# Optimization experiments

Measured on AMD Instinct MI355X. Metric: run time of the kernel, lower is better.

## Reference

```python
import jax, jax.numpy as jnp
import numpy as np

B, S, D, H = 2, 2048, 1024, 16
DH = D // H  # depth per head = 64


def setup_inputs() -> dict:
    key = jax.random.key(0)
    ks = jax.random.split(key, 5)
    sc = 0.02
    return {
        "x": jax.random.normal(ks[0], (B, S, D), dtype=jnp.float32),
        "Wq": jax.random.normal(ks[1], (D, D), dtype=jnp.float32) * sc,
        "bq": jnp.zeros((D,), dtype=jnp.float32),
        "Wk": jax.random.normal(ks[2], (D, D), dtype=jnp.float32) * sc,
        "bk": jnp.zeros((D,), dtype=jnp.float32),
        "Wv": jax.random.normal(ks[3], (D, D), dtype=jnp.float32) * sc,
        "bv": jnp.zeros((D,), dtype=jnp.float32),
        "Wo": jax.random.normal(ks[4], (D, D), dtype=jnp.float32) * sc,
        "bo": jnp.zeros((D,), dtype=jnp.float32),
    }


def _split_heads(t):
    # [B,S,D] -> [B,H,S,DH]
    return t.reshape(B, S, H, DH).transpose(0, 2, 1, 3)


def reference(x, Wq, bq, Wk, bk, Wv, bv, Wo, bo):
    q = _split_heads(x @ Wq + bq)
    k = _split_heads(x @ Wk + bk)
    v = _split_heads(x @ Wv + bv)
    scale = 1.0 / jnp.sqrt(jnp.float32(DH))
    logits = jnp.einsum("bhqd,bhkd->bhqk", q, k) * scale  # [B,H,S,S]
    attn = jax.nn.softmax(logits, axis=-1)
    ctx = jnp.einsum("bhqk,bhkd->bhqd", attn, v)
    ctx = ctx.transpose(0, 2, 1, 3).reshape(B, S, D)
    # dropout is identity at inference
    return ctx @ Wo + bo
```

## Files before the change

kernel.cpp:

```cpp
#include <hip/hip_runtime.h>
#include <hip/hip_bf16.h>

#define S_LEN   2048
#define D_MODEL 1024
#define NHEAD   16
#define DHEAD   64
#define M_ROWS  4096
#define BHEADS  32
#define MEG     1048576

typedef __attribute__((ext_vector_type(8)))  short short8;
typedef __attribute__((ext_vector_type(4)))  float f32x4;
typedef __attribute__((ext_vector_type(16))) float f32x16;
typedef __attribute__((ext_vector_type(4)))  unsigned short us4;
typedef __attribute__((ext_vector_type(2)))  unsigned int uint2v;
typedef __attribute__((ext_vector_type(4)))  unsigned int uint4v;

extern "C" __device__ float __ocml_native_exp2_f32(float);

__device__ __forceinline__ unsigned short f2b(float f) {
    unsigned int u = __builtin_bit_cast(unsigned int, f);
    return (unsigned short)((u + 0x7FFFu + ((u >> 16) & 1u)) >> 16);
}

__device__ __forceinline__ unsigned int cvtpk(float lo, float hi) {
    unsigned int r;
    asm("v_cvt_pk_bf16_f32 %0, %1, %2" : "=v"(r) : "v"(lo), "v"(hi));
    return r;
}

__device__ __forceinline__ float b2f(unsigned short b) {
    return __builtin_bit_cast(float, (unsigned int)b << 16);
}

#define GLOAD16(gp, lp) __builtin_amdgcn_global_load_lds(                     \
        (const __attribute__((address_space(1))) void*)(gp),                  \
        (__attribute__((address_space(3))) void*)(lp), 16, 0, 0)

#define STAGE_OFS(lane) ((((lane) & 3) ^ (((lane) >> 3) & 3)) * 8)

#define ZERO16(v) do { _Pragma("unroll")                                      \
    for (int z_ = 0; z_ < 16; ++z_) (v)[z_] = 0.f; } while (0)

__global__ __launch_bounds__(256) void prep(
    const float* __restrict__ x, unsigned short* __restrict__ xb,
    const float* __restrict__ Wq, const float* __restrict__ Wk,
    const float* __restrict__ Wv, const float* __restrict__ Wo,
    unsigned short* __restrict__ Wqt, unsigned short* __restrict__ Wkt,
    unsigned short* __restrict__ Wvt, unsigned short* __restrict__ Wot)
{
    const int z = blockIdx.z;
    const int tx = threadIdx.x, ty = threadIdx.y;
    if (z == 4) {
        const int blk = blockIdx.y * 32 + blockIdx.x;
        const int base = (blk * 256 + ty * 32 + tx) * 4;
        #pragma unroll
        for (int r = 0; r < 4; ++r) {
            const int i = base + r * (M_ROWS * D_MODEL / 4);
            const float4 v = *(const float4*)&x[i];
            us4 o;
            o.x = f2b(v.x); o.y = f2b(v.y); o.z = f2b(v.z); o.w = f2b(v.w);
            *(us4*)&xb[i] = o;
        }
        return;
    }
    __shared__ float tile[32][33];
    const float* W = z == 0 ? Wq : (z == 1 ? Wk : (z == 2 ? Wv : Wo));
    unsigned short* Wt = z == 0 ? Wqt : (z == 1 ? Wkt : (z == 2 ? Wvt : Wot));
    const int n0 = blockIdx.x * 32, k0 = blockIdx.y * 32;
    #pragma unroll
    for (int i = 0; i < 4; ++i)
        tile[ty + i * 8][tx] = W[(size_t)(k0 + ty + i * 8) * D_MODEL + n0 + tx];
    __syncthreads();
    #pragma unroll
    for (int i = 0; i < 4; ++i)
        Wt[(size_t)(n0 + ty + i * 8) * D_MODEL + k0 + tx] = f2b(tile[tx][ty + i * 8]);
}

__global__ __launch_bounds__(256) void gemm_qkv(
    const unsigned short* __restrict__ xb,
    const unsigned short* __restrict__ Wqt, const unsigned short* __restrict__ Wkt,
    const unsigned short* __restrict__ Wvt,
    const float* __restrict__ bq, const float* __restrict__ bk,
    const float* __restrict__ bv,
    unsigned short* __restrict__ Qb, unsigned short* __restrict__ Kb,
    unsigned short* __restrict__ Vt)
{
    __shared__ unsigned short As[2][128][32];
    __shared__ unsigned short Bs[2][128][32];

    const int id  = (blockIdx.z * 32 + blockIdx.y) * 8 + blockIdx.x;
    const int swz = (id & 7) * 96 + (id >> 3);
    const int z   = swz >> 8;
    const int rem = swz & 255;
    const int bm  = (rem >> 3) * 128;
    const int bn  = (rem & 7) * 128;

    const unsigned short* Wt = z == 0 ? Wqt : (z == 1 ? Wkt : Wvt);
    const float* bias = z == 0 ? bq : (z == 1 ? bk : bv);

    const int t = threadIdx.x, lane = t & 63, w = t >> 6;
    const int wm = w >> 1, wn = w & 1;
    const int lr = lane >> 2, lc = STAGE_OFS(lane);
    const int lm = lane & 15, quad = lane >> 4;
    const int qo = (quad ^ ((lm >> 1) & 3)) * 8;

    f32x4 acc[4][4] = {};

    #pragma unroll
    for (int i = 0; i < 2; ++i) {
        const int c = 2 * w + i;
        GLOAD16(xb + (size_t)(bm + c * 16 + lr) * D_MODEL + lc, &As[0][c * 16][0]);
        GLOAD16(Wt + (size_t)(bn + c * 16 + lr) * D_MODEL + lc, &Bs[0][c * 16][0]);
    }
    __syncthreads();

    for (int it = 0; it < 32; ++it) {
        const int cur = it & 1;
        if (it + 1 < 32) {
            const int kt = (it + 1) * 32;
            #pragma unroll
            for (int i = 0; i < 2; ++i) {
                const int c = 2 * w + i;
                GLOAD16(xb + (size_t)(bm + c * 16 + lr) * D_MODEL + kt + lc,
                        &As[cur ^ 1][c * 16][0]);
                GLOAD16(Wt + (size_t)(bn + c * 16 + lr) * D_MODEL + kt + lc,
                        &Bs[cur ^ 1][c * 16][0]);
            }
        }

        short8 af[4], bfr[4];
        #pragma unroll
        for (int mi = 0; mi < 4; ++mi)
            af[mi] = *(const short8*)&As[cur][wm * 64 + mi * 16 + lm][qo];
        #pragma unroll
        for (int ni = 0; ni < 4; ++ni)
            bfr[ni] = *(const short8*)&Bs[cur][wn * 64 + ni * 16 + lm][qo];
        #pragma unroll
        for (int mi = 0; mi < 4; ++mi)
            #pragma unroll
            for (int ni = 0; ni < 4; ++ni)
                acc[mi][ni] = __builtin_amdgcn_mfma_f32_16x16x32_bf16(
                    af[mi], bfr[ni], acc[mi][ni], 0, 0, 0);

        __syncthreads();
    }

    float bb[4];
    #pragma unroll
    for (int ni = 0; ni < 4; ++ni)
        bb[ni] = bias[bn + wn * 64 + ni * 16 + lm];
    const float scale = (z == 0) ? 0.18033688011112042f : 1.0f;

    if (z < 2) {
        unsigned short* Out = (z == 0) ? Qb : Kb;
        #pragma unroll
        for (int mi = 0; mi < 4; ++mi)
            #pragma unroll
            for (int r = 0; r < 4; ++r) {
                const int row = bm + wm * 64 + mi * 16 + quad * 4 + r;
                const int b = row >> 11, s = row & 2047;
                #pragma unroll
                for (int ni = 0; ni < 4; ++ni) {
                    const int col = bn + wn * 64 + ni * 16 + lm;
                    const int h = col >> 6, d = col & 63;
                    Out[(((size_t)(b * NHEAD + h)) * S_LEN + s) * DHEAD + d] =
                        f2b((acc[mi][ni][r] + bb[ni]) * scale);
                }
            }
    } else {
        #pragma unroll
        for (int mi = 0; mi < 4; ++mi) {
            const int row0 = bm + wm * 64 + mi * 16 + quad * 4;
            const int b = row0 >> 11, s0 = row0 & 2047;
            #pragma unroll
            for (int ni = 0; ni < 4; ++ni) {
                const int col = bn + wn * 64 + ni * 16 + lm;
                const int h = col >> 6, d = col & 63;
                us4 pk;
                pk.x = f2b(acc[mi][ni][0] + bb[ni]);
                pk.y = f2b(acc[mi][ni][1] + bb[ni]);
                pk.z = f2b(acc[mi][ni][2] + bb[ni]);
                pk.w = f2b(acc[mi][ni][3] + bb[ni]);
                *(us4*)&Vt[(((size_t)(b * NHEAD + h)) * DHEAD + d) * S_LEN + s0] = pk;
            }
        }
    }
}

__global__ __launch_bounds__(256) void gemm_out(
    const unsigned short* __restrict__ Ab, const unsigned short* __restrict__ Wot,
    const float* __restrict__ bo, float* __restrict__ out)
{
    __shared__ unsigned short As[2][64][32];
    __shared__ unsigned short Bs[2][128][32];

    const int id  = blockIdx.y * 8 + blockIdx.x;
    const int swz = (id & 7) * 64 + (id >> 3);
    const int bm  = (swz >> 3) * 64;
    const int bn  = (swz & 7) * 128;

    const int t = threadIdx.x, lane = t & 63, w = t >> 6;
    const int wm = w & 1, wn = w >> 1;
    const int lr = lane >> 2, lc = STAGE_OFS(lane);
    const int lm = lane & 15, quad = lane >> 4;
    const int qo = (quad ^ ((lm >> 1) & 3)) * 8;

    f32x4 acc[2][4] = {};

    GLOAD16(Ab + (size_t)(bm + w * 16 + lr) * D_MODEL + lc, &As[0][w * 16][0]);
    #pragma unroll
    for (int i = 0; i < 2; ++i)
        GLOAD16(Wot + (size_t)(bn + w * 32 + i * 16 + lr) * D_MODEL + lc,
                &Bs[0][w * 32 + i * 16][0]);
    __syncthreads();

    for (int it = 0; it < 32; ++it) {
        const int cur = it & 1;
        if (it + 1 < 32) {
            const int kt = (it + 1) * 32;
            GLOAD16(Ab + (size_t)(bm + w * 16 + lr) * D_MODEL + kt + lc,
                    &As[cur ^ 1][w * 16][0]);
            #pragma unroll
            for (int i = 0; i < 2; ++i)
                GLOAD16(Wot + (size_t)(bn + w * 32 + i * 16 + lr) * D_MODEL + kt + lc,
                        &Bs[cur ^ 1][w * 32 + i * 16][0]);
        }

        short8 af[2], bfr[4];
        #pragma unroll
        for (int mi = 0; mi < 2; ++mi)
            af[mi] = *(const short8*)&As[cur][wm * 32 + mi * 16 + lm][qo];
        #pragma unroll
        for (int ni = 0; ni < 4; ++ni)
            bfr[ni] = *(const short8*)&Bs[cur][wn * 64 + ni * 16 + lm][qo];
        #pragma unroll
        for (int mi = 0; mi < 2; ++mi)
            #pragma unroll
            for (int ni = 0; ni < 4; ++ni)
                acc[mi][ni] = __builtin_amdgcn_mfma_f32_16x16x32_bf16(
                    af[mi], bfr[ni], acc[mi][ni], 0, 0, 0);

        __syncthreads();
    }

    float bb[4];
    #pragma unroll
    for (int ni = 0; ni < 4; ++ni)
        bb[ni] = bo[bn + wn * 64 + ni * 16 + lm];

    #pragma unroll
    for (int mi = 0; mi < 2; ++mi)
        #pragma unroll
        for (int r = 0; r < 4; ++r) {
            const int row = bm + wm * 32 + mi * 16 + quad * 4 + r;
            #pragma unroll
            for (int ni = 0; ni < 4; ++ni) {
                const int col = bn + wn * 64 + ni * 16 + lm;
                out[(size_t)row * D_MODEL + col] = acc[mi][ni][r] + bb[ni];
            }
        }
}

__global__ __launch_bounds__(256, 2) void attn_mfma(
    const unsigned short* __restrict__ Q, const unsigned short* __restrict__ K,
    const unsigned short* __restrict__ V, unsigned short* __restrict__ Cx)
{
    __shared__ __align__(16) unsigned char raw[49152];
    unsigned short (*Qs)[128][32] = (unsigned short (*)[128][32])raw;

    const int t = threadIdx.x, lane = t & 63, w = t >> 6;
    const int q5 = lane & 31, hi = lane >> 5;
    const int lr = lane >> 2, lcs = STAGE_OFS(lane);
    const int id  = blockIdx.y * 16 + blockIdx.x;
    const int swz = (id & 7) * 64 + (id >> 3);
    const int q0 = (swz & 15) * 128, bh = swz >> 4;
    const int sw = (q5 >> 1) & 3;
    int sbo[4];
    #pragma unroll
    for (int sb = 0; sb < 4; ++sb) sbo[sb] = (sb ^ sw) * 8;

    const unsigned short* Qh = Q + (size_t)bh * (S_LEN * DHEAD);
    const unsigned short* Kh = K + (size_t)bh * (S_LEN * DHEAD);
    const unsigned short* Vh = V + (size_t)bh * (DHEAD * S_LEN);

    #pragma unroll
    for (int i = 0; i < 2; ++i)
        #pragma unroll
        for (int c = 0; c < 2; ++c)
            GLOAD16(Qh + (size_t)(q0 + w * 32 + c * 16 + lr) * DHEAD + i * 32 + lcs,
                    &Qs[i][w * 32 + c * 16][0]);
    __syncthreads();

    short8 qf[4];
    #pragma unroll
    for (int c = 0; c < 4; ++c)
        qf[c] = *(const short8*)&Qs[c >> 1][w * 32 + q5][sbo[(c & 1) * 2 + hi]];
    __syncthreads();

    short8 onesf;
    #pragma unroll
    for (int j = 0; j < 8; ++j) onesf[j] = (short)0x3F80;

    #define STAGE_KV(IT, BUF) do {                                            \
        const int kt_ = (IT) * 64;                                            \
        unsigned short* ksb_ = (unsigned short*)(raw + (BUF) * 16384);        \
        unsigned short* vsb_ = ksb_ + 4096;                                   \
        _Pragma("unroll")                                                     \
        for (int i_ = 0; i_ < 2; ++i_) {                                      \
            GLOAD16(Kh + (size_t)(kt_ + w * 16 + lr) * DHEAD + i_ * 32 + lcs, \
                    ksb_ + (i_ * 64 + w * 16) * 32);                          \
            GLOAD16(Vh + (size_t)(w * 16 + lr) * S_LEN + kt_ + i_ * 32 + lcs, \
                    vsb_ + (i_ * 64 + w * 16) * 32);                          \
        }                                                                     \
    } while (0)

    #define QK_CHAIN(IT, SF) do {                                             \
        const unsigned short* kn_ = (const unsigned short*)                   \
            (raw + ((IT) % 3) * 16384);                                       \
        _Pragma("unroll")                                                     \
        for (int c_ = 0; c_ < 4; ++c_) {                                      \
            _Pragma("unroll")                                                 \
            for (int mt_ = 0; mt_ < 2; ++mt_) {                               \
                const short8 kf_ = *(const short8*)                           \
                    &kn_[((c_ >> 1) * 64 + mt_ * 32 + q5) * 32                \
                         + sbo[(c_ & 1) * 2 + hi]];                           \
                SF[mt_] = __builtin_amdgcn_mfma_f32_32x32x16_bf16(            \
                    kf_, qf[c_], SF[mt_], 0, 0, 0);                           \
            }                                                                 \
        }                                                                     \
    } while (0)

    f32x16 acc[2];
    f32x16 acc_l;
    ZERO16(acc[0]); ZERO16(acc[1]); ZERO16(acc_l);
    f32x16 sfA[2], sfB[2];

    STAGE_KV(0, 0);
    __syncthreads();
    ZERO16(sfA[0]); ZERO16(sfA[1]);
    QK_CHAIN(0, sfA);
    STAGE_KV(1, 1);

    #define REGION(IT, SFC, SFN, DOQK) do {                                   \
        __syncthreads();                                                      \
        if ((IT) + 2 < 32) STAGE_KV((IT) + 2, ((IT) + 2) % 3);                \
        if (DOQK) {                                                           \
            ZERO16(SFN[0]); ZERO16(SFN[1]);                                   \
            QK_CHAIN((IT) + 1, SFN);                                          \
        }                                                                     \
        const unsigned short* vs_ = (const unsigned short*)                   \
            (raw + ((IT) % 3) * 16384) + 4096;                                \
        _Pragma("unroll")                                                     \
        for (int c = 0; c < 4; ++c) {                                         \
            const int mt = c >> 1, pp = c & 1;                                \
            float p[8];                                                       \
            _Pragma("unroll")                                                 \
            for (int e = 0; e < 8; ++e)                                       \
                p[e] = __ocml_native_exp2_f32(SFC[mt][pp * 8 + e]);           \
            const unsigned int dA = cvtpk(p[0], p[1]);                        \
            const unsigned int dB = cvtpk(p[2], p[3]);                        \
            const unsigned int sA = cvtpk(p[4], p[5]);                        \
            const unsigned int sB = cvtpk(p[6], p[7]);                        \
            const uint2v wA = __builtin_amdgcn_permlane32_swap(dA, sA, false, false); \
            const uint2v wB = __builtin_amdgcn_permlane32_swap(dB, sB, false, false); \
            uint4v wrds;                                                      \
            wrds.x = wA.x; wrds.y = wB.x; wrds.z = wA.y; wrds.w = wB.y;       \
            const short8 pf = __builtin_bit_cast(short8, wrds);               \
            acc_l = __builtin_amdgcn_mfma_f32_32x32x16_bf16(                  \
                pf, onesf, acc_l, 0, 0, 0);                                   \
            _Pragma("unroll")                                                 \
            for (int nt = 0; nt < 2; ++nt) {                                  \
                const short8 vf = *(const short8*)                            \
                    &vs_[((c >> 1) * 64 + nt * 32 + q5) * 32                  \
                         + sbo[(c & 1) * 2 + hi]];                            \
                acc[nt] = __builtin_amdgcn_mfma_f32_32x32x16_bf16(            \
                    pf, vf, acc[nt], 0, 0, 0);                                \
            }                                                                 \
        }                                                                     \
    } while (0)

    for (int itp = 0; itp < 16; ++itp) {
        const int it0 = itp * 2;
        REGION(it0, sfA, sfB, true);
        REGION(it0 + 1, sfB, sfA, (it0 + 2) < 32);
    }
    #undef REGION
    #undef QK_CHAIN
    #undef STAGE_KV

    const int b = bh >> 4, h = bh & 15;
    #pragma unroll
    for (int reg = 0; reg < 16; ++reg) {
        const int row = (reg & 3) + 8 * (reg >> 2) + 4 * hi;
        const float inv = 1.f / acc_l[reg];
        const int q = q0 + w * 32 + row;
        unsigned short* dst = &Cx[((size_t)(b * S_LEN + q)) * D_MODEL + h * 64];
        dst[q5]      = f2b(acc[0][reg] * inv);
        dst[32 + q5] = f2b(acc[1][reg] * inv);
    }
}

extern "C" void kernel_launch(void* const* d_in, const int* in_sizes, int n_in,
                              void* d_out, int out_size, void* d_ws, size_t ws_size,
                              hipStream_t stream)
{
    const float* x  = (const float*)d_in[0];
    const float* Wq = (const float*)d_in[1];
    const float* bq = (const float*)d_in[2];
    const float* Wk = (const float*)d_in[3];
    const float* bk = (const float*)d_in[4];
    const float* Wv = (const float*)d_in[5];
    const float* bv = (const float*)d_in[6];
    const float* Wo = (const float*)d_in[7];
    const float* bo = (const float*)d_in[8];
    float* out = (float*)d_out;

    unsigned short* base = (unsigned short*)d_ws;
    unsigned short* Wot   = base;
    unsigned short* Qb    = base + 1 * MEG;
    unsigned short* Kb    = base + 5 * MEG;
    unsigned short* Vt    = base + 9 * MEG;
    unsigned short* xb    = base + 13 * MEG;
    unsigned short* Wqt   = base + 17 * MEG;
    unsigned short* Wkt   = base + 18 * MEG;
    unsigned short* Wvt   = base + 19 * MEG;
    unsigned short* Cxb   = xb;

    prep<<<dim3(32, 32, 5), dim3(32, 8), 0, stream>>>(
        x, xb, Wq, Wk, Wv, Wo, Wqt, Wkt, Wvt, Wot);

    gemm_qkv<<<dim3(D_MODEL / 128, M_ROWS / 128, 3), dim3(256), 0, stream>>>(
        xb, Wqt, Wkt, Wvt, bq, bk, bv, Qb, Kb, Vt);

    attn_mfma<<<dim3(S_LEN / 128, BHEADS), dim3(256), 0, stream>>>(
        Qb, Kb, Vt, Cxb);

    gemm_out<<<dim3(D_MODEL / 128, M_ROWS / 64), dim3(256), 0, stream>>>(
        Cxb, Wot, bo, out);
}
```

Measured before the change: 191.0 us.

## Fuse Q/K/V projections per block to share the x tile across three weights

The QKV GEMM now has each block compute a 128x64 output tile for all three projections at once, instead of a separate 128x128 tile per projection. Each x tile loaded into shared memory is reused across Wq, Wk and Wv, which cuts global loads of x by a factor of three. The grid drops to 512 blocks with a larger per-block workload, and the epilogue writes one head's worth of columns per projection. In exchange, shared-memory use and accumulator register pressure go up, which may lower occupancy.

```diff
diff --git a/kernel.cpp b/kernel.cpp
--- a/kernel.cpp
+++ b/kernel.cpp
@@ -87,17 +87,15 @@
     unsigned short* __restrict__ Vt)
 {
     __shared__ unsigned short As[2][128][32];
-    __shared__ unsigned short Bs[2][128][32];
-
-    const int id  = (blockIdx.z * 32 + blockIdx.y) * 8 + blockIdx.x;
-    const int swz = (id & 7) * 96 + (id >> 3);
-    const int z   = swz >> 8;
-    const int rem = swz & 255;
-    const int bm  = (rem >> 3) * 128;
-    const int bn  = (rem & 7) * 128;
-
-    const unsigned short* Wt = z == 0 ? Wqt : (z == 1 ? Wkt : Wvt);
-    const float* bias = z == 0 ? bq : (z == 1 ? bk : bv);
+    __shared__ unsigned short Bs[3][2][64][32];
+
+    const int id  = blockIdx.y * 16 + blockIdx.x;
+    const int swz = (id & 7) * 64 + (id >> 3);
+    const int bn  = (swz & 15) * 64;
+    const int bm  = (swz >> 4) * 128;
+
+    const unsigned short* Wt[3] = {Wqt, Wkt, Wvt};
+    const float* bias[3] = {bq, bk, bv};
 
     const int t = threadIdx.x, lane = t & 63, w = t >> 6;
     const int wm = w >> 1, wn = w & 1;
@@ -105,14 +103,16 @@
     const int lm = lane & 15, quad = lane >> 4;
     const int qo = (quad ^ ((lm >> 1) & 3)) * 8;
 
-    f32x4 acc[4][4] = {};
-
-    #pragma unroll
-    for (int i = 0; i < 2; ++i) {
-        const int c = 2 * w + i;
-        GLOAD16(xb + (size_t)(bm + c * 16 + lr) * D_MODEL + lc, &As[0][c * 16][0]);
-        GLOAD16(Wt + (size_t)(bn + c * 16 + lr) * D_MODEL + lc, &Bs[0][c * 16][0]);
-    }
+    f32x4 acc[3][4][2] = {};
+
+    #pragma unroll
+    for (int i = 0; i < 2; ++i)
+        GLOAD16(xb + (size_t)(bm + (2 * w + i) * 16 + lr) * D_MODEL + lc,
+                &As[0][(2 * w + i) * 16][0]);
+    #pragma unroll
+    for (int z = 0; z < 3; ++z)
+        GLOAD16(Wt[z] + (size_t)(bn + w * 16 + lr) * D_MODEL + lc,
+                &Bs[z][0][w * 16][0]);
     __syncthreads();
 
     for (int it = 0; it < 32; ++it) {
@@ -120,69 +120,75 @@
         if (it + 1 < 32) {
             const int kt = (it + 1) * 32;
             #pragma unroll
-            for (int i = 0; i < 2; ++i) {
-                const int c = 2 * w + i;
-                GLOAD16(xb + (size_t)(bm + c * 16 + lr) * D_MODEL + kt + lc,
-                        &As[cur ^ 1][c * 16][0]);
-                GLOAD16(Wt + (size_t)(bn + c * 16 + lr) * D_MODEL + kt + lc,
-                        &Bs[cur ^ 1][c * 16][0]);
-            }
+            for (int i = 0; i < 2; ++i)
+                GLOAD16(xb + (size_t)(bm + (2 * w + i) * 16 + lr) * D_MODEL + kt + lc,
+                        &As[cur ^ 1][(2 * w + i) * 16][0]);
+            #pragma unroll
+            for (int z = 0; z < 3; ++z)
+                GLOAD16(Wt[z] + (size_t)(bn + w * 16 + lr) * D_MODEL + kt + lc,
+                        &Bs[z][cur ^ 1][w * 16][0]);
         }
 
-        short8 af[4], bfr[4];
+        short8 af[4], bfr[3][2];
         #pragma unroll
         for (int mi = 0; mi < 4; ++mi)
             af[mi] = *(const short8*)&As[cur][wm * 64 + mi * 16 + lm][qo];
         #pragma unroll
-        for (int ni = 0; ni < 4; ++ni)
-            bfr[ni] = *(const short8*)&Bs[cur][wn * 64 + ni * 16 + lm][qo];
-        #pragma unroll
-        for (int mi = 0; mi < 4; ++mi)
-            #pragma unroll
-            for (int ni = 0; ni < 4; ++ni)
-                acc[mi][ni] = __builtin_amdgcn_mfma_f32_16x16x32_bf16(
-                    af[mi], bfr[ni], acc[mi][ni], 0, 0, 0);
+        for (int z = 0; z < 3; ++z)
+            #pragma unroll
+            for (int ni = 0; ni < 2; ++ni)
+                bfr[z][ni] = *(const short8*)&Bs[z][cur][wn * 32 + ni * 16 + lm][qo];
+        #pragma unroll
+        for (int z = 0; z < 3; ++z)
+            #pragma unroll
+            for (int mi = 0; mi < 4; ++mi)
+                #pragma unroll
+                for (int ni = 0; ni < 2; ++ni)
+                    acc[z][mi][ni] = __builtin_amdgcn_mfma_f32_16x16x32_bf16(
+                        af[mi], bfr[z][ni], acc[z][mi][ni], 0, 0, 0);
 
         __syncthreads();
     }
 
-    float bb[4];
-    #pragma unroll
-    for (int ni = 0; ni < 4; ++ni)
-        bb[ni] = bias[bn + wn * 64 + ni * 16 + lm];
-    const float scale = (z == 0) ? 0.18033688011112042f : 1.0f;
-
-    if (z < 2) {
-        unsigned short* Out = (z == 0) ? Qb : Kb;
-        #pragma unroll
-        for (int mi = 0; mi < 4; ++mi)
-            #pragma unroll
-            for (int r = 0; r < 4; ++r) {
-                const int row = bm + wm * 64 + mi * 16 + quad * 4 + r;
-                const int b = row >> 11, s = row & 2047;
+    const int h = bn >> 6;
+    #pragma unroll
+    for (int z = 0; z < 3; ++z) {
+        float bb[2];
+        #pragma unroll
+        for (int ni = 0; ni < 2; ++ni)
+            bb[ni] = bias[z][bn + wn * 32 + ni * 16 + lm];
+
+        if (z < 2) {
+            unsigned short* Out = (z == 0) ? Qb : Kb;
+            const float scale = (z == 0) ? 0.18033688011112042f : 1.0f;
+            #pragma unroll
+            for (int mi = 0; mi < 4; ++mi)
                 #pragma unroll
-                for (int ni = 0; ni < 4; ++ni) {
-                    const int col = bn + wn * 64 + ni * 16 + lm;
-                    const int h = col >> 6, d = col & 63;
-                    Out[(((size_t)(b * NHEAD + h)) * S_LEN + s) * DHEAD + d] =
-                        f2b((acc[mi][ni][r] + bb[ni]) * scale);
+                for (int r = 0; r < 4; ++r) {
+                    const int row = bm + wm * 64 + mi * 16 + quad * 4 + r;
+                    const int b = row >> 11, s = row & 2047;
+                    #pragma unroll
+                    for (int ni = 0; ni < 2; ++ni) {
+                        const int d = (bn + wn * 32 + ni * 16 + lm) & 63;
+                        Out[(((size_t)(b * NHEAD + h)) * S_LEN + s) * DHEAD + d] =
+                            f2b((acc[z][mi][ni][r] + bb[ni]) * scale);
+                    }
                 }
-            }
-    } else {
-        #pragma unroll
-        for (int mi = 0; mi < 4; ++mi) {
-            const int row0 = bm + wm * 64 + mi * 16 + quad * 4;
-            const int b = row0 >> 11, s0 = row0 & 2047;
-            #pragma unroll
-            for (int ni = 0; ni < 4; ++ni) {
-                const int col = bn + wn * 64 + ni * 16 + lm;
-                const int h = col >> 6, d = col & 63;
-                us4 pk;
-                pk.x = f2b(acc[mi][ni][0] + bb[ni]);
-                pk.y = f2b(acc[mi][ni][1] + bb[ni]);
-                pk.z = f2b(acc[mi][ni][2] + bb[ni]);
-                pk.w = f2b(acc[mi][ni][3] + bb[ni]);
-                *(us4*)&Vt[(((size_t)(b * NHEAD + h)) * DHEAD + d) * S_LEN + s0] = pk;
+        } else {
+            #pragma unroll
+            for (int mi = 0; mi < 4; ++mi) {
+                const int row0 = bm + wm * 64 + mi * 16 + quad * 4;
+                const int b = row0 >> 11, s0 = row0 & 2047;
+                #pragma unroll
+                for (int ni = 0; ni < 2; ++ni) {
+                    const int d = (bn + wn * 32 + ni * 16 + lm) & 63;
+                    us4 pk;
+                    pk.x = f2b(acc[z][mi][ni][0] + bb[ni]);
+                    pk.y = f2b(acc[z][mi][ni][1] + bb[ni]);
+                    pk.z = f2b(acc[z][mi][ni][2] + bb[ni]);
+                    pk.w = f2b(acc[z][mi][ni][3] + bb[ni]);
+                    *(us4*)&Vt[(((size_t)(b * NHEAD + h)) * DHEAD + d) * S_LEN + s0] = pk;
+                }
             }
         }
     }
@@ -430,7 +436,7 @@
     prep<<<dim3(32, 32, 5), dim3(32, 8), 0, stream>>>(
         x, xb, Wq, Wk, Wv, Wo, Wqt, Wkt, Wvt, Wot);
 
-    gemm_qkv<<<dim3(D_MODEL / 128, M_ROWS / 128, 3), dim3(256), 0, stream>>>(
+    gemm_qkv<<<dim3(16, 32), dim3(256), 0, stream>>>(
         xb, Wqt, Wkt, Wvt, bq, bk, bv, Qb, Kb, Vt);
 
     attn_mfma<<<dim3(S_LEN / 128, BHEADS), dim3(256), 0, stream>>>(
```

Measured after the change: 191.1 us. Within noise of the previous version (+0.1%).
